# Performance work log

Measured on AMD Instinct MI355X. Metric: run time of the kernel, lower is better.

The kernel has to match this reference:

```python
import jax, jax.numpy as jnp
import numpy as np

NLIG = 16384
NPROT = 131072
N = NLIG + NPROT
E = 2097152
B = 256
H = 64


def setup_inputs() -> dict:
    key = jax.random.key(0)
    ks = jax.random.split(key, 40)
    i = iter(range(40))

    def nrm(shape, scale=0.1):
        return (jax.random.normal(ks[next(i)], shape, jnp.float32) * scale)

    inp = {
        'lig_pos': nrm((NLIG, 3), 1.0),
        'lig_feat': nrm((NLIG, 15), 1.0),
        'prot_pos': nrm((NPROT, 3), 1.0),
        'prot_feat': nrm((NPROT, 8), 1.0),
        't': jax.random.uniform(ks[next(i)], (B,), jnp.float32) * 1000.0,
        'lig_batch': jnp.sort(jax.random.randint(ks[next(i)], (NLIG,), 0, B)),
        'prot_batch': jnp.sort(jax.random.randint(ks[next(i)], (NPROT,), 0, B)),
        'edge_index': jax.random.randint(ks[next(i)], (2, E), 0, N),
        'W_lig': nrm((15, H)), 'b_lig': nrm((H,)),
        'W_prot': nrm((8, H)), 'b_prot': nrm((H,)),
        'Wt1': nrm((H, H)), 'bt1': nrm((H,)),
        'Wt2': nrm((H, H)), 'bt2': nrm((H,)),
        'Wrel1': nrm((H, H)), 'brel1': nrm((H,)), 'Wroot1': nrm((H, H)),
        'Wrel2': nrm((H, H)), 'brel2': nrm((H,)), 'Wroot2': nrm((H, H)),
        'Wrel3': nrm((H, H)), 'brel3': nrm((H,)), 'Wroot3': nrm((H, H)),
        'Wro1': nrm((H, H)), 'bro1': nrm((H,)),
        'Wro2': nrm((H, 1)), 'bro2': nrm((1,)),
    }
    return inp


def _time_embedding(t, dim):
    half = dim // 2
    freqs = jnp.exp(jnp.arange(half, dtype=jnp.float32) * (-np.log(10000.0) / (half - 1)))
    e = t[:, None] * freqs[None, :]  # [B, half]
    return jnp.concatenate([jnp.sin(e), jnp.cos(e)], axis=-1)  # [B, dim]


def _silu(x):
    return x * jax.nn.sigmoid(x)


def _graph_conv(x, src, dst, Wrel, brel, Wroot):
    # PyG GraphConv (aggr='add'): lin_rel(sum_j x_j) + lin_root(x)
    agg = jax.ops.segment_sum(x[src], dst, num_segments=N)  # [N, H]
    return agg @ Wrel + brel + x @ Wroot


def reference(lig_pos, lig_feat, prot_pos, prot_feat, t, lig_batch, prot_batch,
              edge_index, W_lig, b_lig, W_prot, b_prot, Wt1, bt1, Wt2, bt2,
              Wrel1, brel1, Wroot1, Wrel2, brel2, Wroot2, Wrel3, brel3, Wroot3,
              Wro1, bro1, Wro2, bro2):
    t_emb = _time_embedding(t, H)                      # [B, H]
    t_emb = _silu(t_emb @ Wt1 + bt1) @ Wt2 + bt2       # time_mlp
    x_lig = lig_feat @ W_lig + b_lig + t_emb[lig_batch]
    x_prot = prot_feat @ W_prot + b_prot
    x = jnp.concatenate([x_lig, x_prot], axis=0)       # [N, H]

    src, dst = edge_index[0], edge_index[1]
    x = _graph_conv(x, src, dst, Wrel1, brel1, Wroot1)
    x = _graph_conv(x, src, dst, Wrel2, brel2, Wroot2)
    x = _graph_conv(x, src, dst, Wrel3, brel3, Wroot3)

    # global_mean_pool over ligand nodes
    lig_x = x[:NLIG]
    sums = jax.ops.segment_sum(lig_x, lig_batch, num_segments=B)  # [B, H]
    cnt = jax.ops.segment_sum(jnp.ones((NLIG,), jnp.float32), lig_batch, num_segments=B)
    pooled = sums / jnp.maximum(cnt, 1.0)[:, None]

    return _silu(pooled @ Wro1 + bro1) @ Wro2 + bro2   # [B, 1]
```

## Files before the change

### kernel.cpp

```cpp
#include <hip/hip_runtime.h>
#include <math.h>

#define NLIG 16384
#define NPROT 131072
#define NTOT (NLIG + NPROT)
#define NEDGE 2097152
#define NB 256
#define H 64
#define NBUCK 576
#define BSHIFT 8
#define BCAP 4608
#define NPW 24

typedef short v4s __attribute__((ext_vector_type(4)));
typedef float v4f __attribute__((ext_vector_type(4)));

__device__ __forceinline__ unsigned short f2bf(float f) {
    unsigned int u = __float_as_uint(f);
    u += 0x7fff + ((u >> 16) & 1);
    return (unsigned short)(u >> 16);
}
__device__ __forceinline__ float bf2f(unsigned short s) {
    return __uint_as_float(((unsigned int)s) << 16);
}
__device__ __forceinline__ float bflo(unsigned int u) {
    return __uint_as_float(u << 16);
}
__device__ __forceinline__ float bfhi(unsigned int u) {
    return __uint_as_float(u & 0xffff0000u);
}

__global__ __launch_bounds__(256) void prep_kernel(const float* __restrict__ t,
                                                   const float* __restrict__ Wt1, const float* __restrict__ bt1,
                                                   const float* __restrict__ Wt2, const float* __restrict__ bt2,
                                                   const float* __restrict__ W0, const float* __restrict__ W1,
                                                   const float* __restrict__ W2, const float* __restrict__ W3,
                                                   const float* __restrict__ W4, const float* __restrict__ W5,
                                                   unsigned short* __restrict__ wbuf,
                                                   float* __restrict__ t_emb,
                                                   unsigned int* __restrict__ bcursor,
                                                   float* __restrict__ pooled) {
    int b = blockIdx.x, tid = threadIdx.x;
    if (b < 96) {
        const float* Ws[6] = {W0, W1, W2, W3, W4, W5};
        int m = b >> 4;
        int tt = (b & 15) * 256 + tid;
        int f = tt >> 8, l = (tt >> 2) & 63, i = tt & 3;
        int kt = f >> 2, ct = f & 3;
        int row = 16 * kt + 4 * (l >> 4) + i;
        int col = 16 * ct + (l & 15);
        wbuf[m * 4096 + tt] = f2bf(Ws[m][row * H + col]);
    } else if (b < 160) {
        __shared__ float emb_s[4][H];
        __shared__ float h1_s[4][H];
        int w = tid >> 6, h = tid & 63;
        int bb = (b - 96) * 4 + w;
        float tv = t[bb];
        int i = h & 31;
        float freq = expf((float)i * (-9.2103403719761836f / 31.0f));
        float e = tv * freq;
        emb_s[w][h] = (h < 32) ? sinf(e) : cosf(e);
        __syncthreads();
        float acc = bt1[h];
        #pragma unroll 8
        for (int k = 0; k < H; k++) acc += emb_s[w][k] * Wt1[k * H + h];
        float sig = 1.0f / (1.0f + expf(-acc));
        h1_s[w][h] = acc * sig;
        __syncthreads();
        float acc2 = bt2[h];
        #pragma unroll 8
        for (int k = 0; k < H; k++) acc2 += h1_s[w][k] * Wt2[k * H + h];
        t_emb[bb * H + h] = acc2;
    } else {
        int idx = (b - 160) * 256 + tid;
        if (idx < NBUCK) bcursor[idx] = 0;
        int idx2 = idx - NBUCK;
        if (idx2 >= 0 && idx2 < NB * H + NB) pooled[idx2] = 0.0f;
    }
}

__global__ void node_init_kernel(const float* __restrict__ lig_feat,
                                 const float* __restrict__ prot_feat,
                                 const int* __restrict__ lig_batch,
                                 const float* __restrict__ t_emb,
                                 const float* __restrict__ W_lig, const float* __restrict__ b_lig,
                                 const float* __restrict__ W_prot, const float* __restrict__ b_prot,
                                 unsigned int* __restrict__ xb) {
    int node = blockIdx.x * 4 + (threadIdx.x >> 6);
    int h = threadIdx.x & 63;
    if (node >= NTOT) return;
    float acc;
    if (node < NLIG) {
        int b = lig_batch[node];
        acc = b_lig[h] + t_emb[b * H + h];
        #pragma unroll
        for (int k = 0; k < 15; k++)
            acc += lig_feat[node * 15 + k] * W_lig[k * H + h];
    } else {
        int p = node - NLIG;
        acc = b_prot[h];
        #pragma unroll
        for (int k = 0; k < 8; k++)
            acc += prot_feat[p * 8 + k] * W_prot[k * H + h];
    }
    float e0 = __shfl(acc, 2 * (h & 31));
    float e1 = __shfl(acc, 2 * (h & 31) + 1);
    if (h < 32)
        xb[node * 32 + h] = (unsigned int)f2bf(e0) | ((unsigned int)f2bf(e1) << 16);
}

__global__ __launch_bounds__(1024) void bucket_fill_kernel(const int* __restrict__ edge_index,
                                                           unsigned int* __restrict__ bcursor,
                                                           unsigned int* __restrict__ bucketed) {
    __shared__ unsigned int lh[NBUCK];
    __shared__ unsigned int lcur[NBUCK];
    __shared__ unsigned int gb[NBUCK];
    int tid = threadIdx.x;
    for (int i = tid; i < NBUCK; i += 1024) lh[i] = 0;
    __syncthreads();
    int e0 = blockIdx.x * 8192;
    int src[8], dst[8];
    #pragma unroll
    for (int k = 0; k < 8; k++) {
        src[k] = edge_index[e0 + k * 1024 + tid];
        dst[k] = edge_index[NEDGE + e0 + k * 1024 + tid];
        atomicAdd(&lh[dst[k] >> BSHIFT], 1);
    }
    __syncthreads();
    if (tid < NBUCK) {
        gb[tid] = atomicAdd(&bcursor[tid], lh[tid]);
        lcur[tid] = 0;
    }
    __syncthreads();
    #pragma unroll
    for (int k = 0; k < 8; k++) {
        int b = dst[k] >> BSHIFT;
        unsigned int r = atomicAdd(&lcur[b], 1);
        unsigned int slot = gb[b] + r;
        if (slot < BCAP)
            bucketed[b * BCAP + slot] = (unsigned int)src[k] | ((unsigned int)(dst[k] & 255) << 18);
    }
}

__global__ __launch_bounds__(1024) void bucket_csr_kernel(const unsigned int* __restrict__ bucketed,
                                                          const unsigned int* __restrict__ bcursor,
                                                          int* __restrict__ off,
                                                          int* __restrict__ ends,
                                                          int* __restrict__ csr_src) {
    __shared__ unsigned int stage[BCAP];
    __shared__ unsigned int lh[256];
    __shared__ unsigned int sc[256];
    __shared__ unsigned int lcur[256];
    int b = blockIdx.x, tid = threadIdx.x;
    unsigned int base = (unsigned int)b * BCAP;
    int cnt = (int)bcursor[b];
    if (cnt > BCAP) cnt = BCAP;
    if (tid < 256) lh[tid] = 0;
    __syncthreads();
    for (int i = tid; i < cnt; i += 1024) {
        unsigned int v = bucketed[base + i];
        stage[i] = v;
        atomicAdd(&lh[v >> 18], 1);
    }
    __syncthreads();
    if (tid < 256) sc[tid] = lh[tid];
    __syncthreads();
    #pragma unroll
    for (int d = 1; d < 256; d <<= 1) {
        unsigned int v = (tid < 256 && tid >= (unsigned)d) ? sc[tid - d] : 0;
        __syncthreads();
        if (tid < 256) sc[tid] += v;
        __syncthreads();
    }
    if (tid < 256) {
        unsigned int excl = sc[tid] - lh[tid];
        lcur[tid] = excl;
        off[b * 256 + tid]  = (int)(base + excl);
        ends[b * 256 + tid] = (int)(base + excl + lh[tid]);
    }
    __syncthreads();
    for (int i = tid; i < cnt; i += 1024) {
        unsigned int v = stage[i];
        unsigned int p = atomicAdd(&lcur[v >> 18], 1);
        csr_src[base + p] = (int)(v & 0x3ffffu);
    }
}

#define ACC8(u)                                   \
    do {                                          \
        a0 += bflo((u).x); a1 += bfhi((u).x);     \
        a2 += bflo((u).y); a3 += bfhi((u).y);     \
        a4 += bflo((u).z); a5 += bfhi((u).z);     \
        a6 += bflo((u).w); a7 += bfhi((u).w);     \
    } while (0)

#define DO_GROUP(BEG, DEG, IDFIRST, AGGROW)                                     \
    {                                                                           \
        int idcur = (IDFIRST);                                                  \
        float a0 = 0.f, a1 = 0.f, a2 = 0.f, a3 = 0.f;                           \
        float a4 = 0.f, a5 = 0.f, a6 = 0.f, a7 = 0.f;                           \
        for (int jb = 0; jb < (DEG); jb += 8) {                                 \
            int idnxt = (jb + 8 + q < (DEG)) ? csr[(BEG) + jb + 8 + q] : -1;    \
            int n0 = __shfl(idcur, s * 8 + 0);                                  \
            int n1 = __shfl(idcur, s * 8 + 1);                                  \
            int n2 = __shfl(idcur, s * 8 + 2);                                  \
            int n3 = __shfl(idcur, s * 8 + 3);                                  \
            int n4 = __shfl(idcur, s * 8 + 4);                                  \
            int n5 = __shfl(idcur, s * 8 + 5);                                  \
            int n6 = __shfl(idcur, s * 8 + 6);                                  \
            int n7 = __shfl(idcur, s * 8 + 7);                                  \
            int c1 = (n1 >= 0) ? n1 : n0;                                       \
            int c2 = (n2 >= 0) ? n2 : n0;                                       \
            int c3 = (n3 >= 0) ? n3 : n0;                                       \
            int c4 = (n4 >= 0) ? n4 : n0;                                       \
            int c5 = (n5 >= 0) ? n5 : n0;                                       \
            int c6 = (n6 >= 0) ? n6 : n0;                                       \
            int c7 = (n7 >= 0) ? n7 : n0;                                       \
            uint4 u0 = *(const uint4*)&xb[n0 * 32 + q * 4];                     \
            uint4 u1 = *(const uint4*)&xb[c1 * 32 + q * 4];                     \
            uint4 u2 = *(const uint4*)&xb[c2 * 32 + q * 4];                     \
            uint4 u3 = *(const uint4*)&xb[c3 * 32 + q * 4];                     \
            uint4 u4 = *(const uint4*)&xb[c4 * 32 + q * 4];                     \
            uint4 u5 = *(const uint4*)&xb[c5 * 32 + q * 4];                     \
            uint4 u6 = *(const uint4*)&xb[c6 * 32 + q * 4];                     \
            uint4 u7 = *(const uint4*)&xb[c7 * 32 + q * 4];                     \
            if (n1 < 0) { u1.x = u1.y = u1.z = u1.w = 0; }                      \
            if (n2 < 0) { u2.x = u2.y = u2.z = u2.w = 0; }                      \
            if (n3 < 0) { u3.x = u3.y = u3.z = u3.w = 0; }                      \
            if (n4 < 0) { u4.x = u4.y = u4.z = u4.w = 0; }                      \
            if (n5 < 0) { u5.x = u5.y = u5.z = u5.w = 0; }                      \
            if (n6 < 0) { u6.x = u6.y = u6.z = u6.w = 0; }                      \
            if (n7 < 0) { u7.x = u7.y = u7.z = u7.w = 0; }                      \
            ACC8(u0); ACC8(u1); ACC8(u2); ACC8(u3);                             \
            ACC8(u4); ACC8(u5); ACC8(u6); ACC8(u7);                             \
            idcur = idnxt;                                                      \
        }                                                                       \
        unsigned int p0 = (unsigned int)f2bf(a0) | ((unsigned int)f2bf(a1) << 16); \
        unsigned int p1 = (unsigned int)f2bf(a2) | ((unsigned int)f2bf(a3) << 16); \
        unsigned int p2 = (unsigned int)f2bf(a4) | ((unsigned int)f2bf(a5) << 16); \
        unsigned int p3 = (unsigned int)f2bf(a6) | ((unsigned int)f2bf(a7) << 16); \
        *(uint4*)&agg_s[(AGGROW) * 72 + q * 8] = make_uint4(p0, p1, p2, p3);    \
    }

__global__ __launch_bounds__(512, 6) void conv_kernel(const int* __restrict__ off,
                                                      const int* __restrict__ ends,
                                                      const int* __restrict__ csr,
                                                      const unsigned int* __restrict__ xb,
                                                      const unsigned short* __restrict__ wbuf,
                                                      const float* __restrict__ brel,
                                                      unsigned int* __restrict__ xob) {
    __shared__ unsigned int wlds[4096];
    __shared__ unsigned short agg_s[8 * NPW * 72];
    const int tid = threadIdx.x;
    const int w = tid >> 6, l = tid & 63;
    const unsigned int* wsrc = (const unsigned int*)wbuf;
    #pragma unroll
    for (int i = 0; i < 8; i++) wlds[i * 512 + tid] = wsrc[i * 512 + tid];

    const int s = l >> 3, q = l & 7;
    const int lrow = l & 15, g16 = l >> 4, g4 = 4 * (l >> 4);
    const int gwid = blockIdx.x * 8 + w;
    const int node0w = gwid * NPW;

    int bvv = (l < NPW) ? off[node0w + l] : 0;
    int evv = (l < NPW) ? ends[node0w + l] : 0;

    int b0 = __shfl(bvv, s),      d0 = __shfl(evv, s) - b0;
    int b1 = __shfl(bvv, 8 + s),  d1 = __shfl(evv, 8 + s) - b1;
    int b2 = __shfl(bvv, 16 + s), d2 = __shfl(evv, 16 + s) - b2;
    int id0 = (q < d0) ? csr[b0 + q] : -1;
    int id1 = (q < d1) ? csr[b1 + q] : -1;
    int id2 = (q < d2) ? csr[b2 + q] : -1;

    __syncthreads();

    float bv[4];
    #pragma unroll
    for (int ct = 0; ct < 4; ct++) bv[ct] = brel[ct * 16 + lrow];

    DO_GROUP(b0, d0, id0, w * NPW + s)
    DO_GROUP(b1, d1, id1, w * NPW + 8 + s)
    DO_GROUP(b2, d2, id2, w * NPW + 16 + s)

    __builtin_amdgcn_wave_barrier();

    v4s ax[4];
    #pragma unroll
    for (int kt = 0; kt < 4; kt++)
        ax[kt] = *(const v4s*)&xb[(node0w + lrow) * 32 + kt * 8 + g16 * 2];
    v4f acc[4];
    #pragma unroll
    for (int ct = 0; ct < 4; ct++) acc[ct] = (v4f){0.f, 0.f, 0.f, 0.f};
    #pragma unroll
    for (int kt = 0; kt < 4; kt++) {
        v4s a_agg = *(const v4s*)&agg_s[(w * NPW + lrow) * 72 + kt * 16 + g4];
        #pragma unroll
        for (int ct = 0; ct < 4; ct++) {
            int f = kt * 4 + ct;
            v4s wr = *(const v4s*)&wlds[f * 128 + l * 2];
            v4s wo = *(const v4s*)&wlds[2048 + f * 128 + l * 2];
            acc[ct] = __builtin_amdgcn_mfma_f32_16x16x16bf16_1k(a_agg, wr, acc[ct], 0, 0, 0);
            acc[ct] = __builtin_amdgcn_mfma_f32_16x16x16bf16_1k(ax[kt], wo, acc[ct], 0, 0, 0);
        }
    }
    const int r2row = 16 + (l & 7);
    v4s ax2[4];
    #pragma unroll
    for (int kt = 0; kt < 4; kt++)
        ax2[kt] = *(const v4s*)&xb[(node0w + r2row) * 32 + kt * 8 + g16 * 2];
    v4f acc2[4];
    #pragma unroll
    for (int ct = 0; ct < 4; ct++) acc2[ct] = (v4f){0.f, 0.f, 0.f, 0.f};
    #pragma unroll
    for (int kt = 0; kt < 4; kt++) {
        v4s a_agg2 = *(const v4s*)&agg_s[(w * NPW + r2row) * 72 + kt * 16 + g4];
        #pragma unroll
        for (int ct = 0; ct < 4; ct++) {
            int f = kt * 4 + ct;
            v4s wr = *(const v4s*)&wlds[f * 128 + l * 2];
            v4s wo = *(const v4s*)&wlds[2048 + f * 128 + l * 2];
            acc2[ct] = __builtin_amdgcn_mfma_f32_16x16x16bf16_1k(a_agg2, wr, acc2[ct], 0, 0, 0);
            acc2[ct] = __builtin_amdgcn_mfma_f32_16x16x16bf16_1k(ax2[kt], wo, acc2[ct], 0, 0, 0);
        }
    }
    __builtin_amdgcn_wave_barrier();

    #pragma unroll
    for (int ct = 0; ct < 4; ct++) {
        #pragma unroll
        for (int r = 0; r < 4; r++)
            agg_s[(w * NPW + g4 + r) * 72 + ct * 16 + lrow] = f2bf(acc[ct][r] + bv[ct]);
    }
    if (g16 < 2) {
        #pragma unroll
        for (int ct = 0; ct < 4; ct++) {
            #pragma unroll
            for (int r = 0; r < 4; r++)
                agg_s[(w * NPW + 16 + g4 + r) * 72 + ct * 16 + lrow] =
                    f2bf(acc2[ct][r] + bv[ct]);
        }
    }
    __builtin_amdgcn_wave_barrier();

    {
        int row = l >> 2, qq = l & 3;
        const unsigned int* srcp = (const unsigned int*)&agg_s[(w * NPW + row) * 72 + qq * 16];
        uint4 v0 = *(const uint4*)(srcp);
        uint4 v1 = *(const uint4*)(srcp + 4);
        *(uint4*)&xob[(node0w + row) * 32 + qq * 8] = v0;
        *(uint4*)&xob[(node0w + row) * 32 + qq * 8 + 4] = v1;
    }
    {
        int row = 16 + (l >> 3), qq = l & 7;
        *(uint4*)&xob[(node0w + row) * 32 + qq * 4] =
            *(const uint4*)&agg_s[(w * NPW + row) * 72 + qq * 8];
    }
}

__global__ __launch_bounds__(512, 6) void conv_lig_kernel(const int* __restrict__ off,
                                                          const int* __restrict__ ends,
                                                          const int* __restrict__ csr,
                                                          const unsigned int* __restrict__ xb,
                                                          const unsigned short* __restrict__ wbuf,
                                                          const float* __restrict__ brel,
                                                          const int* __restrict__ lig_batch,
                                                          float* __restrict__ pooled,
                                                          float* __restrict__ cnt) {
    __shared__ unsigned int wlds[4096];
    __shared__ unsigned short agg_s[8 * 8 * 72];
    const int tid = threadIdx.x;
    const int w = tid >> 6, l = tid & 63;
    const unsigned int* wsrc = (const unsigned int*)wbuf;
    #pragma unroll
    for (int i = 0; i < 8; i++) wlds[i * 512 + tid] = wsrc[i * 512 + tid];

    const int s = l >> 3, q = l & 7;
    const int lrow = l & 15, g16 = l >> 4, g4 = 4 * (l >> 4);
    const int gwid = blockIdx.x * 8 + w;
    const int node0w = gwid * 8;

    int bvv = (l < 8) ? off[node0w + l] : 0;
    int evv = (l < 8) ? ends[node0w + l] : 0;
    int b0 = __shfl(bvv, s), d0 = __shfl(evv, s) - b0;
    int id0 = (q < d0) ? csr[b0 + q] : -1;

    __syncthreads();

    float bv[4];
    #pragma unroll
    for (int ct = 0; ct < 4; ct++) bv[ct] = brel[ct * 16 + lrow];

    DO_GROUP(b0, d0, id0, w * 8 + s)

    __builtin_amdgcn_wave_barrier();

    const int arow = lrow & 7;
    v4s ax[4];
    #pragma unroll
    for (int kt = 0; kt < 4; kt++)
        ax[kt] = *(const v4s*)&xb[(node0w + arow) * 32 + kt * 8 + g16 * 2];
    v4f acc[4];
    #pragma unroll
    for (int ct = 0; ct < 4; ct++) acc[ct] = (v4f){0.f, 0.f, 0.f, 0.f};
    #pragma unroll
    for (int kt = 0; kt < 4; kt++) {
        v4s a_agg = *(const v4s*)&agg_s[(w * 8 + arow) * 72 + kt * 16 + g4];
        #pragma unroll
        for (int ct = 0; ct < 4; ct++) {
            int f = kt * 4 + ct;
            v4s wr = *(const v4s*)&wlds[f * 128 + l * 2];
            v4s wo = *(const v4s*)&wlds[2048 + f * 128 + l * 2];
            acc[ct] = __builtin_amdgcn_mfma_f32_16x16x16bf16_1k(a_agg, wr, acc[ct], 0, 0, 0);
            acc[ct] = __builtin_amdgcn_mfma_f32_16x16x16bf16_1k(ax[kt], wo, acc[ct], 0, 0, 0);
        }
    }

    if (g16 < 2) {
        #pragma unroll
        for (int r = 0; r < 4; r++) {
            int node = node0w + g4 + r;
            int bb = lig_batch[node];
            #pragma unroll
            for (int ct = 0; ct < 4; ct++)
                unsafeAtomicAdd(&pooled[bb * H + ct * 16 + lrow], acc[ct][r] + bv[ct]);
            if (lrow == 0) unsafeAtomicAdd(&cnt[bb], 1.0f);
        }
    }
}

__global__ void readout_kernel(const float* __restrict__ pooled, const float* __restrict__ cnt,
                               const float* __restrict__ Wro1, const float* __restrict__ bro1,
                               const float* __restrict__ Wro2, const float* __restrict__ bro2,
                               float* __restrict__ out) {
    __shared__ float pm[4][H];
    int w = threadIdx.x >> 6;
    int h = threadIdx.x & 63;
    int b = blockIdx.x * 4 + w;
    float c = fmaxf(cnt[b], 1.0f);
    pm[w][h] = pooled[b * H + h] / c;
    __syncthreads();
    float acc = bro1[h];
    #pragma unroll 8
    for (int k = 0; k < H; k++) acc += pm[w][k] * Wro1[k * H + h];
    float sig = 1.0f / (1.0f + expf(-acc));
    float s = acc * sig;
    float r = s * Wro2[h];
    #pragma unroll
    for (int off = 32; off; off >>= 1) r += __shfl_down(r, off);
    if (h == 0) out[b] = r + bro2[0];
}

extern "C" void kernel_launch(void* const* d_in, const int* in_sizes, int n_in,
                              void* d_out, int out_size, void* d_ws, size_t ws_size,
                              hipStream_t stream) {
    const float* lig_feat  = (const float*)d_in[1];
    const float* prot_feat = (const float*)d_in[3];
    const float* t         = (const float*)d_in[4];
    const int*   lig_batch = (const int*)d_in[5];
    const int*   edge_index= (const int*)d_in[7];
    const float* W_lig  = (const float*)d_in[8];
    const float* b_lig  = (const float*)d_in[9];
    const float* W_prot = (const float*)d_in[10];
    const float* b_prot = (const float*)d_in[11];
    const float* Wt1 = (const float*)d_in[12];
    const float* bt1 = (const float*)d_in[13];
    const float* Wt2 = (const float*)d_in[14];
    const float* bt2 = (const float*)d_in[15];
    const float* Wrel[3]  = {(const float*)d_in[16], (const float*)d_in[19], (const float*)d_in[22]};
    const float* brel[3]  = {(const float*)d_in[17], (const float*)d_in[20], (const float*)d_in[23]};
    const float* Wroot[3] = {(const float*)d_in[18], (const float*)d_in[21], (const float*)d_in[24]};
    const float* Wro1 = (const float*)d_in[25];
    const float* bro1 = (const float*)d_in[26];
    const float* Wro2 = (const float*)d_in[27];
    const float* bro2 = (const float*)d_in[28];
    float* out = (float*)d_out;

    char* ws = (char*)d_ws;
    int*            off_a   = (int*)(ws);
    int*            ends_a  = (int*)(ws + 655360);
    unsigned int*   bcursor = (unsigned int*)(ws + 1310720);
    float*          t_emb   = (float*)(ws + 1376256);
    float*          pooled  = (float*)(ws + 1441792);
    float*          cnt     = (float*)(ws + 1507328);
    unsigned short* wbuf    = (unsigned short*)(ws + 1572864);
    int*            csr_src = (int*)(ws + 2097152);
    unsigned int*   bucketed= (unsigned int*)(ws + 14680064);
    unsigned int*   xb0     = (unsigned int*)(ws + 27262976);
    unsigned int*   xb1     = (unsigned int*)(ws + 46137344);

    prep_kernel<<<228, 256, 0, stream>>>(t, Wt1, bt1, Wt2, bt2,
                                         Wrel[0], Wroot[0], Wrel[1], Wroot[1], Wrel[2], Wroot[2],
                                         wbuf, t_emb, bcursor, pooled);

    node_init_kernel<<<NTOT / 4, 256, 0, stream>>>(lig_feat, prot_feat, lig_batch, t_emb,
                                                   W_lig, b_lig, W_prot, b_prot, xb0);

    bucket_fill_kernel<<<NEDGE / 8192, 1024, 0, stream>>>(edge_index, bcursor, bucketed);
    bucket_csr_kernel<<<NBUCK, 1024, 0, stream>>>(bucketed, bcursor, off_a, ends_a, csr_src);

    conv_kernel<<<768, 512, 0, stream>>>(off_a, ends_a, csr_src, xb0,
                                         wbuf, brel[0], xb1);
    conv_kernel<<<768, 512, 0, stream>>>(off_a, ends_a, csr_src, xb1,
                                         wbuf + 8192, brel[1], xb0);
    conv_lig_kernel<<<NLIG / 64, 512, 0, stream>>>(off_a, ends_a, csr_src, xb0,
                                                   wbuf + 16384, brel[2], lig_batch,
                                                   pooled, cnt);

    readout_kernel<<<NB / 4, 256, 0, stream>>>(pooled, cnt, Wro1, bro1, Wro2, bro2, out);
}
```

Measured before the change: 222.1 us.

## Merge preprocessing kernels into two multi-role launches and stage CSR in LDS

```diff
diff --git a/kernel.cpp b/kernel.cpp
--- a/kernel.cpp
+++ b/kernel.cpp
@@ -30,31 +30,61 @@
     return __uint_as_float(u & 0xffff0000u);
 }
 
-__global__ __launch_bounds__(256) void prep_kernel(const float* __restrict__ t,
-                                                   const float* __restrict__ Wt1, const float* __restrict__ bt1,
-                                                   const float* __restrict__ Wt2, const float* __restrict__ bt2,
-                                                   const float* __restrict__ W0, const float* __restrict__ W1,
-                                                   const float* __restrict__ W2, const float* __restrict__ W3,
-                                                   const float* __restrict__ W4, const float* __restrict__ W5,
-                                                   unsigned short* __restrict__ wbuf,
-                                                   float* __restrict__ t_emb,
-                                                   unsigned int* __restrict__ bcursor,
-                                                   float* __restrict__ pooled) {
+__global__ __launch_bounds__(1024) void megaA_kernel(const int* __restrict__ edge_index,
+                                                     unsigned int* __restrict__ bcursor,
+                                                     unsigned int* __restrict__ bucketed,
+                                                     const float* __restrict__ t,
+                                                     const float* __restrict__ Wt1, const float* __restrict__ bt1,
+                                                     const float* __restrict__ Wt2, const float* __restrict__ bt2,
+                                                     const float* __restrict__ W0, const float* __restrict__ W1,
+                                                     const float* __restrict__ W2, const float* __restrict__ W3,
+                                                     const float* __restrict__ W4, const float* __restrict__ W5,
+                                                     unsigned short* __restrict__ wbuf,
+                                                     float* __restrict__ t_emb) {
+    __shared__ unsigned int lh[NBUCK];
+    __shared__ unsigned int lcur[NBUCK];
+    __shared__ unsigned int gb[NBUCK];
+    __shared__ float emb_s[16][H];
+    __shared__ float h1_s[16][H];
     int b = blockIdx.x, tid = threadIdx.x;
-    if (b < 96) {
+    if (b < 256) {
+        for (int i = tid; i < NBUCK; i += 1024) lh[i] = 0;
+        __syncthreads();
+        int e0 = b * 8192;
+        int src[8], dst[8];
+        #pragma unroll
+        for (int k = 0; k < 8; k++) {
+            src[k] = edge_index[e0 + k * 1024 + tid];
+            dst[k] = edge_index[NEDGE + e0 + k * 1024 + tid];
+            atomicAdd(&lh[dst[k] >> BSHIFT], 1);
+        }
+        __syncthreads();
+        if (tid < NBUCK) {
+            gb[tid] = atomicAdd(&bcursor[tid], lh[tid]);
+            lcur[tid] = 0;
+        }
+        __syncthreads();
+        #pragma unroll
+        for (int k = 0; k < 8; k++) {
+            int bb = dst[k] >> BSHIFT;
+            unsigned int r = atomicAdd(&lcur[bb], 1);
+            unsigned int slot = gb[bb] + r;
+            if (slot < BCAP)
+                bucketed[bb * BCAP + slot] =
+                    (unsigned int)src[k] | ((unsigned int)(dst[k] & 255) << 18);
+        }
+    } else if (b < 280) {
         const float* Ws[6] = {W0, W1, W2, W3, W4, W5};
-        int m = b >> 4;
-        int tt = (b & 15) * 256 + tid;
+        int tglob = (b - 256) * 1024 + tid;
+        int m = tglob >> 12, tt = tglob & 4095;
         int f = tt >> 8, l = (tt >> 2) & 63, i = tt & 3;
         int kt = f >> 2, ct = f & 3;
         int row = 16 * kt + 4 * (l >> 4) + i;
         int col = 16 * ct + (l & 15);
         wbuf[m * 4096 + tt] = f2bf(Ws[m][row * H + col]);
-    } else if (b < 160) {
-        __shared__ float emb_s[4][H];
-        __shared__ float h1_s[4][H];
+    } else {
         int w = tid >> 6, h = tid & 63;
-        int bb = (b - 96) * 4 + w;
+        int bb = (b - 280) * 16 + w;
         float tv = t[bb];
         int i = h & 31;
         float freq = expf((float)i * (-9.2103403719761836f / 31.0f));
@@ -71,118 +101,86 @@
         #pragma unroll 8
         for (int k = 0; k < H; k++) acc2 += h1_s[w][k] * Wt2[k * H + h];
         t_emb[bb * H + h] = acc2;
-    } else {
-        int idx = (b - 160) * 256 + tid;
-        if (idx < NBUCK) bcursor[idx] = 0;
-        int idx2 = idx - NBUCK;
-        if (idx2 >= 0 && idx2 < NB * H + NB) pooled[idx2] = 0.0f;
-    }
-}
-
-__global__ void node_init_kernel(const float* __restrict__ lig_feat,
-                                 const float* __restrict__ prot_feat,
-                                 const int* __restrict__ lig_batch,
-                                 const float* __restrict__ t_emb,
-                                 const float* __restrict__ W_lig, const float* __restrict__ b_lig,
-                                 const float* __restrict__ W_prot, const float* __restrict__ b_prot,
-                                 unsigned int* __restrict__ xb) {
-    int node = blockIdx.x * 4 + (threadIdx.x >> 6);
-    int h = threadIdx.x & 63;
-    if (node >= NTOT) return;
-    float acc;
-    if (node < NLIG) {
-        int b = lig_batch[node];
-        acc = b_lig[h] + t_emb[b * H + h];
-        #pragma unroll
-        for (int k = 0; k < 15; k++)
-            acc += lig_feat[node * 15 + k] * W_lig[k * H + h];
-    } else {
-        int p = node - NLIG;
-        acc = b_prot[h];
-        #pragma unroll
-        for (int k = 0; k < 8; k++)
-            acc += prot_feat[p * 8 + k] * W_prot[k * H + h];
-    }
-    float e0 = __shfl(acc, 2 * (h & 31));
-    float e1 = __shfl(acc, 2 * (h & 31) + 1);
-    if (h < 32)
-        xb[node * 32 + h] = (unsigned int)f2bf(e0) | ((unsigned int)f2bf(e1) << 16);
-}
-
-__global__ __launch_bounds__(1024) void bucket_fill_kernel(const int* __restrict__ edge_index,
-                                                           unsigned int* __restrict__ bcursor,
-                                                           unsigned int* __restrict__ bucketed) {
-    __shared__ unsigned int lh[NBUCK];
-    __shared__ unsigned int lcur[NBUCK];
-    __shared__ unsigned int gb[NBUCK];
-    int tid = threadIdx.x;
-    for (int i = tid; i < NBUCK; i += 1024) lh[i] = 0;
-    __syncthreads();
-    int e0 = blockIdx.x * 8192;
-    int src[8], dst[8];
-    #pragma unroll
-    for (int k = 0; k < 8; k++) {
-        src[k] = edge_index[e0 + k * 1024 + tid];
-        dst[k] = edge_index[NEDGE + e0 + k * 1024 + tid];
-        atomicAdd(&lh[dst[k] >> BSHIFT], 1);
-    }
-    __syncthreads();
-    if (tid < NBUCK) {
-        gb[tid] = atomicAdd(&bcursor[tid], lh[tid]);
-        lcur[tid] = 0;
-    }
-    __syncthreads();
-    #pragma unroll
-    for (int k = 0; k < 8; k++) {
-        int b = dst[k] >> BSHIFT;
-        unsigned int r = atomicAdd(&lcur[b], 1);
-        unsigned int slot = gb[b] + r;
-        if (slot < BCAP)
-            bucketed[b * BCAP + slot] = (unsigned int)src[k] | ((unsigned int)(dst[k] & 255) << 18);
-    }
-}
-
-__global__ __launch_bounds__(1024) void bucket_csr_kernel(const unsigned int* __restrict__ bucketed,
-                                                          const unsigned int* __restrict__ bcursor,
-                                                          int* __restrict__ off,
-                                                          int* __restrict__ ends,
-                                                          int* __restrict__ csr_src) {
+    }
+}
+
+__global__ __launch_bounds__(1024) void megaB_kernel(const unsigned int* __restrict__ bucketed,
+                                                     const unsigned int* __restrict__ bcursor,
+                                                     int* __restrict__ off,
+                                                     int* __restrict__ ends,
+                                                     int* __restrict__ csr_src,
+                                                     const float* __restrict__ lig_feat,
+                                                     const float* __restrict__ prot_feat,
+                                                     const int* __restrict__ lig_batch,
+                                                     const float* __restrict__ t_emb,
+                                                     const float* __restrict__ W_lig,
+                                                     const float* __restrict__ b_lig,
+                                                     const float* __restrict__ W_prot,
+                                                     const float* __restrict__ b_prot,
+                                                     unsigned int* __restrict__ xb) {
     __shared__ unsigned int stage[BCAP];
+    __shared__ unsigned int csr_l[BCAP];
     __shared__ unsigned int lh[256];
     __shared__ unsigned int sc[256];
     __shared__ unsigned int lcur[256];
     int b = blockIdx.x, tid = threadIdx.x;
-    unsigned int base = (unsigned int)b * BCAP;
-    int cnt = (int)bcursor[b];
-    if (cnt > BCAP) cnt = BCAP;
-    if (tid < 256) lh[tid] = 0;
-    __syncthreads();
-    for (int i = tid; i < cnt; i += 1024) {
-        unsigned int v = bucketed[base + i];
-        stage[i] = v;
-        atomicAdd(&lh[v >> 18], 1);
-    }
-    __syncthreads();
-    if (tid < 256) sc[tid] = lh[tid];
-    __syncthreads();
-    #pragma unroll
-    for (int d = 1; d < 256; d <<= 1) {
-        unsigned int v = (tid < 256 && tid >= (unsigned)d) ? sc[tid - d] : 0;
-        __syncthreads();
-        if (tid < 256) sc[tid] += v;
-        __syncthreads();
-    }
-    if (tid < 256) {
-        unsigned int excl = sc[tid] - lh[tid];
-        lcur[tid] = excl;
-        off[b * 256 + tid]  = (int)(base + excl);
-        ends[b * 256 + tid] = (int)(base + excl + lh[tid]);
-    }
-    __syncthreads();
-    for (int i = tid; i < cnt; i += 1024) {
-        unsigned int v = stage[i];
-        unsigned int p = atomicAdd(&lcur[v >> 18], 1);
-        csr_src[base + p] = (int)(v & 0x3ffffu);
+    if (b < NBUCK) {
+        unsigned int base = (unsigned int)b * BCAP;
+        int cnt = (int)bcursor[b];
+        if (cnt > BCAP) cnt = BCAP;
+        if (tid < 256) lh[tid] = 0;
+        __syncthreads();
+        for (int i = tid; i < cnt; i += 1024) {
+            unsigned int v = bucketed[base + i];
+            stage[i] = v;
+            atomicAdd(&lh[v >> 18], 1);
+        }
+        __syncthreads();
+        if (tid < 256) sc[tid] = lh[tid];
+        __syncthreads();
+        #pragma unroll
+        for (int d = 1; d < 256; d <<= 1) {
+            unsigned int v = (tid < 256 && tid >= (unsigned)d) ? sc[tid - d] : 0;
+            __syncthreads();
+            if (tid < 256) sc[tid] += v;
+            __syncthreads();
+        }
+        if (tid < 256) {
+            unsigned int excl = sc[tid] - lh[tid];
+            lcur[tid] = excl;
+            off[b * 256 + tid]  = (int)(base + excl);
+            ends[b * 256 + tid] = (int)(base + excl + lh[tid]);
+        }
+        __syncthreads();
+        for (int i = tid; i < cnt; i += 1024) {
+            unsigned int v = stage[i];
+            unsigned int p = atomicAdd(&lcur[v >> 18], 1);
+            csr_l[p] = v & 0x3ffffu;
+        }
+        __syncthreads();
+        for (int i = tid; i < cnt; i += 1024)
+            csr_src[base + i] = (int)csr_l[i];
+    } else {
+        int node = (b - NBUCK) * 16 + (tid >> 6);
+        int h = tid & 63;
+        float acc;
+        if (node < NLIG) {
+            int bb = lig_batch[node];
+            acc = b_lig[h] + t_emb[bb * H + h];
+            #pragma unroll
+            for (int k = 0; k < 15; k++)
+                acc += lig_feat[node * 15 + k] * W_lig[k * H + h];
+        } else {
+            int p = node - NLIG;
+            acc = b_prot[h];
+            #pragma unroll
+            for (int k = 0; k < 8; k++)
+                acc += prot_feat[p * 8 + k] * W_prot[k * H + h];
+        }
+        float e0 = __shfl(acc, 2 * (h & 31));
+        float e1 = __shfl(acc, 2 * (h & 31) + 1);
+        if (h < 32)
+            xb[node * 32 + h] = (unsigned int)f2bf(e0) | ((unsigned int)f2bf(e1) << 16);
     }
 }
 
@@ -479,24 +477,26 @@
     int*            off_a   = (int*)(ws);
     int*            ends_a  = (int*)(ws + 655360);
     unsigned int*   bcursor = (unsigned int*)(ws + 1310720);
-    float*          t_emb   = (float*)(ws + 1376256);
-    float*          pooled  = (float*)(ws + 1441792);
-    float*          cnt     = (float*)(ws + 1507328);
+    float*          pooled  = (float*)(ws + 1313024);
+    float*          cnt     = (float*)(ws + 1378560);
+    float*          t_emb   = (float*)(ws + 1380352);
     unsigned short* wbuf    = (unsigned short*)(ws + 1572864);
     int*            csr_src = (int*)(ws + 2097152);
     unsigned int*   bucketed= (unsigned int*)(ws + 14680064);
     unsigned int*   xb0     = (unsigned int*)(ws + 27262976);
     unsigned int*   xb1     = (unsigned int*)(ws + 46137344);
 
-    prep_kernel<<<228, 256, 0, stream>>>(t, Wt1, bt1, Wt2, bt2,
-                                         Wrel[0], Wroot[0], Wrel[1], Wroot[1], Wrel[2], Wroot[2],
-                                         wbuf, t_emb, bcursor, pooled);
-
-    node_init_kernel<<<NTOT / 4, 256, 0, stream>>>(lig_feat, prot_feat, lig_batch, t_emb,
-                                                   W_lig, b_lig, W_prot, b_prot, xb0);
-
-    bucket_fill_kernel<<<NEDGE / 8192, 1024, 0, stream>>>(edge_index, bcursor, bucketed);
-    bucket_csr_kernel<<<NBUCK, 1024, 0, stream>>>(bucketed, bcursor, off_a, ends_a, csr_src);
+    hipMemsetAsync(bcursor, 0, 68864, stream);
+
+    megaA_kernel<<<296, 1024, 0, stream>>>(edge_index, bcursor, bucketed,
+                                           t, Wt1, bt1, Wt2, bt2,
+                                           Wrel[0], Wroot[0], Wrel[1], Wroot[1], Wrel[2], Wroot[2],
+                                           wbuf, t_emb);
+
+    megaB_kernel<<<NBUCK + NTOT / 16, 1024, 0, stream>>>(bucketed, bcursor,
+                                                         off_a, ends_a, csr_src,
+                                                         lig_feat, prot_feat, lig_batch, t_emb,
+                                                         W_lig, b_lig, W_prot, b_prot, xb0);
 
     conv_kernel<<<768, 512, 0, stream>>>(off_a, ends_a, csr_src, xb0,
                                          wbuf, brel[0], xb1);
```

Result: faster. 213.7 us (-3.8%).
